# Performance work log

Measured on AMD Instinct MI355X. Metric: run time of the kernel, lower is better.

## Reference

```python
import jax, jax.numpy as jnp
import numpy as np

DIM = 1024


def setup_inputs() -> dict:
    key = jax.random.key(0)
    kx, kw = jax.random.split(key)
    x = jax.random.normal(kx, (4, 2048, DIM), dtype=jnp.float32)
    # fused qkv projection weight, torch Linear convention: [out_features, in_features]
    W_qkv = jax.random.normal(kw, (3 * DIM, DIM), dtype=jnp.float32) * (DIM ** -0.5)
    return {"x": x, "W_qkv": W_qkv}


def reference(x, W_qkv):
    # fused QKV projection: y = x @ W^T -> [B, N, 3*DIM]
    qkv = jnp.einsum('bnd,ed->bne', x, W_qkv)
    B, N, _ = qkv.shape
    # rearrange 'b n (e d) -> e b n d' with e=3
    qkv = qkv.reshape(B, N, 3, DIM).transpose(2, 0, 1, 3)
    q, k, v = qkv[0], qkv[1], qkv[2]
    scale = DIM ** (-0.5)  # note: scale uses full dim, module never splits heads
    attn = jnp.einsum('bnd,bmd->bnm', q * scale, k)  # [B, N, N]
    attn = jax.nn.softmax(attn, axis=-1)
    out = jnp.einsum('bnm,bmd->bnd', attn, v)
    return out
```

## Files before the change

kernel.cpp:

```cpp
#include <hip/hip_runtime.h>

using half8   = __attribute__((ext_vector_type(8))) _Float16;
using f32x4   = __attribute__((ext_vector_type(4))) float;
using ushort8 = __attribute__((ext_vector_type(8))) unsigned short;

__device__ __forceinline__ void gload16(const void* g, void* l) {
  __builtin_amdgcn_global_load_lds(
      (const __attribute__((address_space(1))) void*)g,
      (__attribute__((address_space(3))) void*)l, 16, 0, 0);
}

__device__ __forceinline__ void xcd_swizzle(int& x, int& y, int& z) {
  const int gx = gridDim.x, gy = gridDim.y;
  const int nwg = gx * gy * gridDim.z;
  const int f = blockIdx.x + gx * (blockIdx.y + gy * blockIdx.z);
  const int w = (f & 7) * (nwg >> 3) + (f >> 3);
  const int r = w >> 5, u = w & 31;
  const int nrx = gx >> 3, nry = gy >> 2;
  const int pz  = nrx * nry;
  const int rz  = r / pz, rr = r % pz;
  x = (rr % nrx) * 8 + (u & 7);
  y = (rr / nrx) * 4 + (u >> 3);
  z = rz;
}

__global__ __launch_bounds__(256) void cast_f32_f16(
    const float* __restrict__ in, unsigned short* __restrict__ out, long n) {
  long i = ((long)blockIdx.x * 256 + threadIdx.x) * 8;
  if (i >= n) return;
  float4 a = *(const float4*)(in + i);
  float4 b = *(const float4*)(in + i + 4);
  union { _Float16 h[8]; ushort8 u; } r;
  r.h[0] = (_Float16)a.x; r.h[1] = (_Float16)a.y;
  r.h[2] = (_Float16)a.z; r.h[3] = (_Float16)a.w;
  r.h[4] = (_Float16)b.x; r.h[5] = (_Float16)b.y;
  r.h[6] = (_Float16)b.z; r.h[7] = (_Float16)b.w;
  *(ushort8*)(out + i) = r.u;
}

template <int MODE>
__global__ __launch_bounds__(256, 2) void gemm4w(
    const unsigned short* __restrict__ Ab, const unsigned short* __restrict__ Bb,
    int K, int lda, int ldb, long sA, long sB,
    void* __restrict__ o0, void* __restrict__ o1, void* __restrict__ o2) {
  constexpr int ASZ = 128 * 64;
  constexpr int BSZ = 128 * 64;
  __shared__ unsigned short lds[2 * ASZ + 2 * BSZ];

  const int tid  = threadIdx.x;
  const int lane = tid & 63;
  const int wv   = tid >> 6;
  const int wr   = wv >> 1, wc = wv & 1;
  const int fr   = lane & 15, fq = lane >> 4;
  int bxi, byi, bzi;
  xcd_swizzle(bxi, byi, bzi);
  const int bm = byi * 128;
  const int bn = bxi * 128;
  const int bz = bzi;

  const unsigned short* A = Ab + (long)bz * sA;
  const unsigned short* B = Bb + (long)bz * sB;

  const int row_s = tid >> 3;
  const int col_s = ((tid & 7) ^ (row_s & 7)) * 8;
  const unsigned short* aS = A + (long)(bm + row_s) * lda + col_s;
  const unsigned short* bS = B + (long)(bn + row_s) * ldb + col_s;
  unsigned short* ldsA = lds;
  unsigned short* ldsB = lds + 2 * ASZ;

  const int kg0 = ((0 * 4 + fq) ^ (fr & 7)) * 16;
  const int kg1 = ((1 * 4 + fq) ^ (fr & 7)) * 16;
  const int aRd = (wr * 64 + fr) * 128;
  const int bRd = (wc * 64 + fr) * 128;

  f32x4 acc[4][4] = {};
  half8 bf[4][2];
  half8 a0[2], a1[2], a2[2], a3[2];

  const int nt = K / 64;

#define STAGE_T(SL, T)                                                             \
  {                                                                                \
    const long kt = (long)(T) * 64;                                                \
    unsigned short* dA = ldsA + (SL) * ASZ + wv * 512;                             \
    unsigned short* dB = ldsB + (SL) * BSZ + wv * 512;                             \
    _Pragma("unroll") for (int i = 0; i < 4; ++i)                                  \
      gload16(aS + (long)(i * 32) * lda + kt, dA + i * 2048);                      \
    _Pragma("unroll") for (int i = 0; i < 4; ++i)                                  \
      gload16(bS + (long)(i * 32) * ldb + kt, dB + i * 2048);                      \
  }
#define RDA(DST, MI)                                                               \
  DST[0] = *(const half8*)(lA + aRd + (MI) * 2048 + kg0);                          \
  DST[1] = *(const half8*)(lA + aRd + (MI) * 2048 + kg1);
#define MFMAQ(MI, AA)                                                              \
  __builtin_amdgcn_s_setprio(1);                                                   \
  _Pragma("unroll") for (int ks = 0; ks < 2; ++ks)                                 \
  _Pragma("unroll") for (int ni = 0; ni < 4; ++ni)                                 \
    acc[MI][ni] = __builtin_amdgcn_mfma_f32_16x16x32_f16(                          \
        AA[ks], bf[ni][ks], acc[MI][ni], 0, 0, 0);                                 \
  __builtin_amdgcn_s_setprio(0);

  STAGE_T(0, 0)
  asm volatile("s_waitcnt vmcnt(0)" ::: "memory");
  __builtin_amdgcn_s_barrier();
  __builtin_amdgcn_sched_barrier(0);

  for (int t = 0; t < nt; ++t) {
    const int s = t & 1;
    const char* lA = (const char*)(ldsA + s * ASZ);
    const char* lB = (const char*)(ldsB + s * BSZ);
#pragma unroll
    for (int ni = 0; ni < 4; ++ni) {
      bf[ni][0] = *(const half8*)(lB + bRd + ni * 2048 + kg0);
      bf[ni][1] = *(const half8*)(lB + bRd + ni * 2048 + kg1);
    }
    RDA(a0, 0)
    RDA(a1, 1)
    if (t + 1 < nt) STAGE_T(s ^ 1, t + 1)
    MFMAQ(0, a0)
    RDA(a2, 2)
    MFMAQ(1, a1)
    RDA(a3, 3)
    MFMAQ(2, a2)
    MFMAQ(3, a3)
    asm volatile("s_waitcnt vmcnt(0)" ::: "memory");
    __builtin_amdgcn_s_barrier();
    __builtin_amdgcn_sched_barrier(0);
  }
#undef STAGE_T
#undef RDA
#undef MFMAQ

  const int row0 = bm + wr * 64 + fq * 4;
  const int col0 = bn + wc * 64 + fr;
#pragma unroll
  for (int mi = 0; mi < 4; ++mi) {
#pragma unroll
    for (int ni = 0; ni < 4; ++ni) {
      f32x4 c = acc[mi][ni];
      const long r0 = row0 + mi * 16;
      const long e  = col0 + ni * 16;
      if constexpr (MODE == 0) {
        _Float16* q  = (_Float16*)o0;
        _Float16* kk = (_Float16*)o1;
        _Float16* vv = (_Float16*)o2;
#pragma unroll
        for (int j = 0; j < 4; ++j) {
          const long i = r0 + j;
          const float val = c[j];
          if (e < 1024)      q [i * 1024 + e]          = (_Float16)(val * 0.03125f);
          else if (e < 2048) kk[i * 1024 + (e - 1024)] = (_Float16)val;
          else               vv[i * 1024 + (e - 2048)] = (_Float16)val;
        }
      } else if constexpr (MODE == 1) {
        float* C = (float*)o0 + (long)bz * 2048 * 2048;
#pragma unroll
        for (int j = 0; j < 4; ++j) C[(r0 + j) * 2048 + e] = c[j];
      } else {
        float* C = (float*)o0 + (long)bz * 2048 * 1024;
#pragma unroll
        for (int j = 0; j < 4; ++j) C[(r0 + j) * 1024 + e] = c[j];
      }
    }
  }
}

__global__ __launch_bounds__(256) void transpose_v(
    const unsigned short* __restrict__ v, unsigned short* __restrict__ vT) {
  __shared__ unsigned short t[64][72];
  const long b = blockIdx.z;
  const unsigned short* vb = v + b * (2048L * 1024);
  unsigned short* ob = vT + b * (1024L * 2048);
  const int n0 = blockIdx.y * 64;
  const int d0 = blockIdx.x * 64;
  const int tid = threadIdx.x;
  const int r  = tid >> 2;
  const int c0 = (tid & 3) * 16;
  const unsigned short* src = vb + (long)(n0 + r) * 1024 + d0 + c0;
  *(ushort4*)&t[r][c0]      = *(const ushort4*)(src);
  *(ushort4*)&t[r][c0 + 4]  = *(const ushort4*)(src + 4);
  *(ushort4*)&t[r][c0 + 8]  = *(const ushort4*)(src + 8);
  *(ushort4*)&t[r][c0 + 12] = *(const ushort4*)(src + 12);
  __syncthreads();
  union { unsigned short h[8]; ushort8 u; } w0, w1;
#pragma unroll
  for (int j = 0; j < 8; ++j) w0.h[j] = t[c0 + j][r];
#pragma unroll
  for (int j = 0; j < 8; ++j) w1.h[j] = t[c0 + 8 + j][r];
  unsigned short* dst = ob + (long)(d0 + r) * 2048 + n0 + c0;
  *(ushort8*)dst       = w0.u;
  *(ushort8*)(dst + 8) = w1.u;
}

__global__ __launch_bounds__(256) void softmax_rows(float* __restrict__ S) {
  const long row = blockIdx.x;
  float* p = S + row * 2048;
  const int t = threadIdx.x;
  float4 v0 = *(const float4*)(p + t * 8);
  float4 v1 = *(const float4*)(p + t * 8 + 4);
  float f[8] = {v0.x, v0.y, v0.z, v0.w, v1.x, v1.y, v1.z, v1.w};
  float m = f[0];
#pragma unroll
  for (int j = 1; j < 8; ++j) m = fmaxf(m, f[j]);
  for (int o = 32; o; o >>= 1) m = fmaxf(m, __shfl_xor(m, o));
  __shared__ float redm[4];
  if (!(t & 63)) redm[t >> 6] = m;
  __syncthreads();
  m = fmaxf(fmaxf(redm[0], redm[1]), fmaxf(redm[2], redm[3]));
  float e[8], s = 0.f;
#pragma unroll
  for (int j = 0; j < 8; ++j) { e[j] = __expf(f[j] - m); s += e[j]; }
  for (int o = 32; o; o >>= 1) s += __shfl_xor(s, o);
  __shared__ float reds[4];
  if (!(t & 63)) reds[t >> 6] = s;
  __syncthreads();
  s = reds[0] + reds[1] + reds[2] + reds[3];
  const float inv = 1.0f / s;
  union { _Float16 h[8]; ushort8 u; } r;
#pragma unroll
  for (int j = 0; j < 8; ++j) r.h[j] = (_Float16)(e[j] * inv);
  *(ushort8*)((unsigned short*)p + t * 8) = r.u;
}

extern "C" void kernel_launch(void* const* d_in, const int* in_sizes, int n_in,
                              void* d_out, int out_size, void* d_ws, size_t ws_size,
                              hipStream_t stream) {
  const float* x = (const float*)d_in[0];
  const float* W = (const float*)d_in[1];
  float* out = (float*)d_out;
  char* ws = (char*)d_ws;

  const long MB16 = 16777216;
  unsigned short* q  = (unsigned short*)(ws);
  unsigned short* k  = (unsigned short*)(ws + MB16);
  unsigned short* vT = (unsigned short*)(ws + 2 * MB16);
  float*          S  = (float*)(ws + 3 * MB16);
  unsigned short* xb = (unsigned short*)(ws + 3 * MB16);
  unsigned short* wb = (unsigned short*)(ws + 4 * MB16);
  unsigned short* v  = (unsigned short*)(ws + 4 * MB16 + 6291456);

  cast_f32_f16<<<4096, 256, 0, stream>>>(x, xb, 8388608L);
  cast_f32_f16<<<1536, 256, 0, stream>>>(W, wb, 3145728L);
  gemm4w<0><<<dim3(24, 64, 1), 256, 0, stream>>>(
      xb, wb, 1024, 1024, 1024, 0L, 0L, q, k, v);
  transpose_v<<<dim3(16, 32, 4), 256, 0, stream>>>(v, vT);
  gemm4w<1><<<dim3(16, 16, 4), 256, 0, stream>>>(
      q, k, 1024, 1024, 1024, 2048L * 1024, 2048L * 1024, S, nullptr, nullptr);
  softmax_rows<<<8192, 256, 0, stream>>>(S);
  gemm4w<2><<<dim3(8, 16, 4), 256, 0, stream>>>(
      (unsigned short*)S, vT, 2048, 4096, 2048, 2048L * 4096, 1024L * 2048,
      out, nullptr, nullptr);
}
```

Baseline: 171.2 us.

## Load GEMM B operand directly from global into double-buffered registers

```diff
diff --git a/kernel.cpp b/kernel.cpp
--- a/kernel.cpp
+++ b/kernel.cpp
@@ -39,13 +39,12 @@
 }
 
 template <int MODE>
-__global__ __launch_bounds__(256, 2) void gemm4w(
+__global__ __launch_bounds__(256, 2) void gemm_bd(
     const unsigned short* __restrict__ Ab, const unsigned short* __restrict__ Bb,
     int K, int lda, int ldb, long sA, long sB,
     void* __restrict__ o0, void* __restrict__ o1, void* __restrict__ o2) {
   constexpr int ASZ = 128 * 64;
-  constexpr int BSZ = 128 * 64;
-  __shared__ unsigned short lds[2 * ASZ + 2 * BSZ];
+  __shared__ unsigned short ldsA[2 * ASZ];
 
   const int tid  = threadIdx.x;
   const int lane = tid & 63;
@@ -64,70 +63,81 @@
   const int row_s = tid >> 3;
   const int col_s = ((tid & 7) ^ (row_s & 7)) * 8;
   const unsigned short* aS = A + (long)(bm + row_s) * lda + col_s;
-  const unsigned short* bS = B + (long)(bn + row_s) * ldb + col_s;
-  unsigned short* ldsA = lds;
-  unsigned short* ldsB = lds + 2 * ASZ;
 
   const int kg0 = ((0 * 4 + fq) ^ (fr & 7)) * 16;
   const int kg1 = ((1 * 4 + fq) ^ (fr & 7)) * 16;
   const int aRd = (wr * 64 + fr) * 128;
-  const int bRd = (wc * 64 + fr) * 128;
+
+  const unsigned short* bR0 = B + (long)(bn + wc * 64 + 0  + fr) * ldb + fq * 8;
+  const unsigned short* bR1 = B + (long)(bn + wc * 64 + 16 + fr) * ldb + fq * 8;
+  const unsigned short* bR2 = B + (long)(bn + wc * 64 + 32 + fr) * ldb + fq * 8;
+  const unsigned short* bR3 = B + (long)(bn + wc * 64 + 48 + fr) * ldb + fq * 8;
 
   f32x4 acc[4][4] = {};
-  half8 bf[4][2];
+  half8 bfA[4][2], bfB[4][2];
   half8 a0[2], a1[2], a2[2], a3[2];
 
   const int nt = K / 64;
 
-#define STAGE_T(SL, T)                                                             \
+#define LOADB(DST, T)                                                              \
   {                                                                                \
-    const long kt = (long)(T) * 64;                                                \
-    unsigned short* dA = ldsA + (SL) * ASZ + wv * 512;                             \
-    unsigned short* dB = ldsB + (SL) * BSZ + wv * 512;                             \
+    const long ktb = (long)(T) * 64;                                               \
+    DST[0][0] = *(const half8*)(bR0 + ktb);                 \
+    DST[0][1] = *(const half8*)(bR0 + ktb + 32);            \
+    DST[1][0] = *(const half8*)(bR1 + ktb);                                        \
+    DST[1][1] = *(const half8*)(bR1 + ktb + 32);                                   \
+    DST[2][0] = *(const half8*)(bR2 + ktb);                                        \
+    DST[2][1] = *(const half8*)(bR2 + ktb + 32);                                   \
+    DST[3][0] = *(const half8*)(bR3 + ktb);                                        \
+    DST[3][1] = *(const half8*)(bR3 + ktb + 32);                                   \
+  }
+#define STAGE_A(SL, T)                                                             \
+  {                                                                                \
+    const long kta = (long)(T) * 64;                                               \
+    unsigned short* d = ldsA + (SL) * ASZ + wv * 512;                              \
     _Pragma("unroll") for (int i = 0; i < 4; ++i)                                  \
-      gload16(aS + (long)(i * 32) * lda + kt, dA + i * 2048);                      \
-    _Pragma("unroll") for (int i = 0; i < 4; ++i)                                  \
-      gload16(bS + (long)(i * 32) * ldb + kt, dB + i * 2048);                      \
+      gload16(aS + (long)(i * 32) * lda + kta, d + i * 2048);                      \
   }
 #define RDA(DST, MI)                                                               \
   DST[0] = *(const half8*)(lA + aRd + (MI) * 2048 + kg0);                          \
   DST[1] = *(const half8*)(lA + aRd + (MI) * 2048 + kg1);
-#define MFMAQ(MI, AA)                                                              \
+#define MFMAQ(MI, AA, BF)                                                          \
   __builtin_amdgcn_s_setprio(1);                                                   \
   _Pragma("unroll") for (int ks = 0; ks < 2; ++ks)                                 \
   _Pragma("unroll") for (int ni = 0; ni < 4; ++ni)                                 \
     acc[MI][ni] = __builtin_amdgcn_mfma_f32_16x16x32_f16(                          \
-        AA[ks], bf[ni][ks], acc[MI][ni], 0, 0, 0);                                 \
+        AA[ks], BF[ni][ks], acc[MI][ni], 0, 0, 0);                                 \
   __builtin_amdgcn_s_setprio(0);
 
-  STAGE_T(0, 0)
-  asm volatile("s_waitcnt vmcnt(0)" ::: "memory");
-  __builtin_amdgcn_s_barrier();
-  __builtin_amdgcn_sched_barrier(0);
-
-  for (int t = 0; t < nt; ++t) {
-    const int s = t & 1;
-    const char* lA = (const char*)(ldsA + s * ASZ);
-    const char* lB = (const char*)(ldsB + s * BSZ);
-#pragma unroll
-    for (int ni = 0; ni < 4; ++ni) {
-      bf[ni][0] = *(const half8*)(lB + bRd + ni * 2048 + kg0);
-      bf[ni][1] = *(const half8*)(lB + bRd + ni * 2048 + kg1);
-    }
-    RDA(a0, 0)
-    RDA(a1, 1)
-    if (t + 1 < nt) STAGE_T(s ^ 1, t + 1)
-    MFMAQ(0, a0)
-    RDA(a2, 2)
-    MFMAQ(1, a1)
-    RDA(a3, 3)
-    MFMAQ(2, a2)
-    MFMAQ(3, a3)
-    asm volatile("s_waitcnt vmcnt(0)" ::: "memory");
-    __builtin_amdgcn_s_barrier();
-    __builtin_amdgcn_sched_barrier(0);
-  }
-#undef STAGE_T
+#define TILE_BODY(T, BC, BN_)                                                      \
+  {                                                                                \
+    const int tcur = (T);                                                          \
+    const int sl = tcur & 1;                                                       \
+    const char* lA = (const char*)(ldsA + sl * ASZ);                               \
+    if (tcur + 1 < nt) LOADB(BN_, tcur + 1)    \
+    RDA(a0, 0)                                                                     \
+    RDA(a1, 1)                                                                     \
+    if (tcur + 1 < nt) STAGE_A(sl ^ 1, tcur + 1)                                   \
+    MFMAQ(0, a0, BC)                                                               \
+    RDA(a2, 2)                                                                     \
+    MFMAQ(1, a1, BC)                                                               \
+    RDA(a3, 3)                                                                     \
+    MFMAQ(2, a2, BC)                                                               \
+    MFMAQ(3, a3, BC)                                                               \
+    __syncthreads();                                                               \
+  }
+
+  STAGE_A(0, 0)
+  LOADB(bfA, 0)
+  __syncthreads();
+
+  for (int tt = 0; tt < nt; tt += 2) {
+    TILE_BODY(tt, bfA, bfB)
+    TILE_BODY(tt + 1, bfB, bfA)
+  }
+#undef TILE_BODY
+#undef LOADB
+#undef STAGE_A
 #undef RDA
 #undef MFMAQ
 
@@ -241,13 +251,13 @@
 
   cast_f32_f16<<<4096, 256, 0, stream>>>(x, xb, 8388608L);
   cast_f32_f16<<<1536, 256, 0, stream>>>(W, wb, 3145728L);
-  gemm4w<0><<<dim3(24, 64, 1), 256, 0, stream>>>(
+  gemm_bd<0><<<dim3(24, 64, 1), 256, 0, stream>>>(
       xb, wb, 1024, 1024, 1024, 0L, 0L, q, k, v);
   transpose_v<<<dim3(16, 32, 4), 256, 0, stream>>>(v, vT);
-  gemm4w<1><<<dim3(16, 16, 4), 256, 0, stream>>>(
+  gemm_bd<1><<<dim3(16, 16, 4), 256, 0, stream>>>(
       q, k, 1024, 1024, 1024, 2048L * 1024, 2048L * 1024, S, nullptr, nullptr);
   softmax_rows<<<8192, 256, 0, stream>>>(S);
-  gemm4w<2><<<dim3(8, 16, 4), 256, 0, stream>>>(
+  gemm_bd<2><<<dim3(8, 16, 4), 256, 0, stream>>>(
       (unsigned short*)S, vT, 2048, 4096, 2048, 2048L * 4096, 1024L * 2048,
       out, nullptr, nullptr);
 }
```

Measured after the change: 303.1 us. 1.77x slower.

## Switch GEMM inner loop from 16x16x32 to 32x32x16 MFMA tiles

Applied to the files above, without the earlier changes.

```diff
diff --git a/kernel.cpp b/kernel.cpp
--- a/kernel.cpp
+++ b/kernel.cpp
@@ -1,7 +1,7 @@
 #include <hip/hip_runtime.h>
 
 using half8   = __attribute__((ext_vector_type(8))) _Float16;
-using f32x4   = __attribute__((ext_vector_type(4))) float;
+using f32x16  = __attribute__((ext_vector_type(16))) float;
 using ushort8 = __attribute__((ext_vector_type(8))) unsigned short;
 
 __device__ __forceinline__ void gload16(const void* g, void* l) {
@@ -39,7 +39,7 @@
 }
 
 template <int MODE>
-__global__ __launch_bounds__(256, 2) void gemm4w(
+__global__ __launch_bounds__(256, 2) void gemm32(
     const unsigned short* __restrict__ Ab, const unsigned short* __restrict__ Bb,
     int K, int lda, int ldb, long sA, long sB,
     void* __restrict__ o0, void* __restrict__ o1, void* __restrict__ o2) {
@@ -51,7 +51,7 @@
   const int lane = tid & 63;
   const int wv   = tid >> 6;
   const int wr   = wv >> 1, wc = wv & 1;
-  const int fr   = lane & 15, fq = lane >> 4;
+  const int lr   = lane & 31, lh = lane >> 5;
   int bxi, byi, bzi;
   xcd_swizzle(bxi, byi, bzi);
   const int bm = byi * 128;
@@ -68,14 +68,16 @@
   unsigned short* ldsA = lds;
   unsigned short* ldsB = lds + 2 * ASZ;
 
-  const int kg0 = ((0 * 4 + fq) ^ (fr & 7)) * 16;
-  const int kg1 = ((1 * 4 + fq) ^ (fr & 7)) * 16;
-  const int aRd = (wr * 64 + fr) * 128;
-  const int bRd = (wc * 64 + fr) * 128;
-
-  f32x4 acc[4][4] = {};
-  half8 bf[4][2];
-  half8 a0[2], a1[2], a2[2], a3[2];
+  const int kg0 = ((0 + lh) ^ (lr & 7)) * 16;
+  const int kg1 = ((2 + lh) ^ (lr & 7)) * 16;
+  const int kg2 = ((4 + lh) ^ (lr & 7)) * 16;
+  const int kg3 = ((6 + lh) ^ (lr & 7)) * 16;
+  const int aRd = (wr * 64 + lr) * 128;
+  const int bRd = (wc * 64 + lr) * 128;
+
+  f32x16 acc[2][2] = {};
+  half8 bf[2][4];
+  half8 aF0, aF1, aF2, aF3;
 
   const int nt = K / 64;
 
@@ -89,77 +91,78 @@
     _Pragma("unroll") for (int i = 0; i < 4; ++i)                                  \
       gload16(bS + (long)(i * 32) * ldb + kt, dB + i * 2048);                      \
   }
-#define RDA(DST, MI)                                                               \
-  DST[0] = *(const half8*)(lA + aRd + (MI) * 2048 + kg0);                          \
-  DST[1] = *(const half8*)(lA + aRd + (MI) * 2048 + kg1);
-#define MFMAQ(MI, AA)                                                              \
-  __builtin_amdgcn_s_setprio(1);                                                   \
-  _Pragma("unroll") for (int ks = 0; ks < 2; ++ks)                                 \
-  _Pragma("unroll") for (int ni = 0; ni < 4; ++ni)                                 \
-    acc[MI][ni] = __builtin_amdgcn_mfma_f32_16x16x32_f16(                          \
-        AA[ks], bf[ni][ks], acc[MI][ni], 0, 0, 0);                                 \
-  __builtin_amdgcn_s_setprio(0);
+#define RDA(MI)                                                                    \
+  aF0 = *(const half8*)(lA + aRd + (MI) * 4096 + kg0);                             \
+  aF1 = *(const half8*)(lA + aRd + (MI) * 4096 + kg1);                             \
+  aF2 = *(const half8*)(lA + aRd + (MI) * 4096 + kg2);                             \
+  aF3 = *(const half8*)(lA + aRd + (MI) * 4096 + kg3);
+#define MFMAT(MI)                                                                  \
+  _Pragma("unroll") for (int ni = 0; ni < 2; ++ni) {                               \
+    acc[MI][ni] = __builtin_amdgcn_mfma_f32_32x32x16_f16(aF0, bf[ni][0],           \
+                                                         acc[MI][ni], 0, 0, 0);   \
+    acc[MI][ni] = __builtin_amdgcn_mfma_f32_32x32x16_f16(aF1, bf[ni][1],           \
+                                                         acc[MI][ni], 0, 0, 0);   \
+    acc[MI][ni] = __builtin_amdgcn_mfma_f32_32x32x16_f16(aF2, bf[ni][2],           \
+                                                         acc[MI][ni], 0, 0, 0);   \
+    acc[MI][ni] = __builtin_amdgcn_mfma_f32_32x32x16_f16(aF3, bf[ni][3],           \
+                                                         acc[MI][ni], 0, 0, 0);   \
+  }
 
   STAGE_T(0, 0)
   asm volatile("s_waitcnt vmcnt(0)" ::: "memory");
   __builtin_amdgcn_s_barrier();
   __builtin_amdgcn_sched_barrier(0);
 
-  for (int t = 0; t < nt; ++t) {
-    const int s = t & 1;
-    const char* lA = (const char*)(ldsA + s * ASZ);
-    const char* lB = (const char*)(ldsB + s * BSZ);
-#pragma unroll
-    for (int ni = 0; ni < 4; ++ni) {
-      bf[ni][0] = *(const half8*)(lB + bRd + ni * 2048 + kg0);
-      bf[ni][1] = *(const half8*)(lB + bRd + ni * 2048 + kg1);
+  for (int tt = 0; tt < nt; ++tt) {
+    const int sl = tt & 1;
+    const char* lA = (const char*)(ldsA + sl * ASZ);
+    const char* lB = (const char*)(ldsB + sl * BSZ);
+#pragma unroll
+    for (int ni = 0; ni < 2; ++ni) {
+      bf[ni][0] = *(const half8*)(lB + bRd + ni * 4096 + kg0);
+      bf[ni][1] = *(const half8*)(lB + bRd + ni * 4096 + kg1);
+      bf[ni][2] = *(const half8*)(lB + bRd + ni * 4096 + kg2);
+      bf[ni][3] = *(const half8*)(lB + bRd + ni * 4096 + kg3);
     }
-    RDA(a0, 0)
-    RDA(a1, 1)
-    if (t + 1 < nt) STAGE_T(s ^ 1, t + 1)
-    MFMAQ(0, a0)
-    RDA(a2, 2)
-    MFMAQ(1, a1)
-    RDA(a3, 3)
-    MFMAQ(2, a2)
-    MFMAQ(3, a3)
+    RDA(0)
+    if (tt + 1 < nt) STAGE_T(sl ^ 1, tt + 1)
+    MFMAT(0)
+    RDA(1)
+    MFMAT(1)
     asm volatile("s_waitcnt vmcnt(0)" ::: "memory");
     __builtin_amdgcn_s_barrier();
     __builtin_amdgcn_sched_barrier(0);
   }
 #undef STAGE_T
 #undef RDA
-#undef MFMAQ
-
-  const int row0 = bm + wr * 64 + fq * 4;
-  const int col0 = bn + wc * 64 + fr;
-#pragma unroll
-  for (int mi = 0; mi < 4; ++mi) {
-#pragma unroll
-    for (int ni = 0; ni < 4; ++ni) {
-      f32x4 c = acc[mi][ni];
-      const long r0 = row0 + mi * 16;
-      const long e  = col0 + ni * 16;
-      if constexpr (MODE == 0) {
-        _Float16* q  = (_Float16*)o0;
-        _Float16* kk = (_Float16*)o1;
-        _Float16* vv = (_Float16*)o2;
-#pragma unroll
-        for (int j = 0; j < 4; ++j) {
-          const long i = r0 + j;
-          const float val = c[j];
+#undef MFMAT
+
+  const int row0 = bm + wr * 64 + lh * 4;
+  const int col0 = bn + wc * 64 + lr;
+#pragma unroll
+  for (int mi = 0; mi < 2; ++mi) {
+#pragma unroll
+    for (int ni = 0; ni < 2; ++ni) {
+      f32x16 c = acc[mi][ni];
+      const long e = col0 + ni * 32;
+#pragma unroll
+      for (int reg = 0; reg < 16; ++reg) {
+        const long i = row0 + mi * 32 + (reg & 3) + 8 * (reg >> 2);
+        const float val = c[reg];
+        if constexpr (MODE == 0) {
+          _Float16* q  = (_Float16*)o0;
+          _Float16* kk = (_Float16*)o1;
+          _Float16* vv = (_Float16*)o2;
           if (e < 1024)      q [i * 1024 + e]          = (_Float16)(val * 0.03125f);
           else if (e < 2048) kk[i * 1024 + (e - 1024)] = (_Float16)val;
           else               vv[i * 1024 + (e - 2048)] = (_Float16)val;
+        } else if constexpr (MODE == 1) {
+          float* C = (float*)o0 + (long)bz * 2048 * 2048;
+          C[i * 2048 + e] = val;
+        } else {
+          float* C = (float*)o0 + (long)bz * 2048 * 1024;
+          C[i * 1024 + e] = val;
         }
-      } else if constexpr (MODE == 1) {
-        float* C = (float*)o0 + (long)bz * 2048 * 2048;
-#pragma unroll
-        for (int j = 0; j < 4; ++j) C[(r0 + j) * 2048 + e] = c[j];
-      } else {
-        float* C = (float*)o0 + (long)bz * 2048 * 1024;
-#pragma unroll
-        for (int j = 0; j < 4; ++j) C[(r0 + j) * 1024 + e] = c[j];
       }
     }
   }
@@ -241,13 +244,13 @@
 
   cast_f32_f16<<<4096, 256, 0, stream>>>(x, xb, 8388608L);
   cast_f32_f16<<<1536, 256, 0, stream>>>(W, wb, 3145728L);
-  gemm4w<0><<<dim3(24, 64, 1), 256, 0, stream>>>(
+  gemm32<0><<<dim3(24, 64, 1), 256, 0, stream>>>(
       xb, wb, 1024, 1024, 1024, 0L, 0L, q, k, v);
   transpose_v<<<dim3(16, 32, 4), 256, 0, stream>>>(v, vT);
-  gemm4w<1><<<dim3(16, 16, 4), 256, 0, stream>>>(
+  gemm32<1><<<dim3(16, 16, 4), 256, 0, stream>>>(
       q, k, 1024, 1024, 1024, 2048L * 1024, 2048L * 1024, S, nullptr, nullptr);
   softmax_rows<<<8192, 256, 0, stream>>>(S);
-  gemm4w<2><<<dim3(8, 16, 4), 256, 0, stream>>>(
+  gemm32<2><<<dim3(8, 16, 4), 256, 0, stream>>>(
       (unsigned short*)S, vT, 2048, 4096, 2048, 2048L * 4096, 1024L * 2048,
       out, nullptr, nullptr);
 }
```

After: 190.4 us. 1.11x slower.
